# Performance work log

Measured on AMD Instinct MI355X. Metric: run time of the kernel, lower is better.

Reference implementation:

```python
import jax, jax.numpy as jnp
import numpy as np

B, N, C_IN = 128, 49, 2048   # batch, spatial tokens, backbone channels
G, D, H = 256, 768, 8        # query groups, decoder dim, heads
FF = 2048                    # feedforward dim
NUM_CLASSES = 12547
DUP = 50                     # int(12547/256 + 0.999)


def setup_inputs() -> dict:
    key = jax.random.key(0)
    ks = jax.random.split(key, 24)

    def rn(k, shape, std):
        return jax.random.normal(k, shape, dtype=jnp.float32) * std

    inp = {
        "x": rn(ks[0], (B, N, C_IN), 1.0),
        # embed_standart: Linear(2048 -> 768)
        "W_embed": rn(ks[1], (C_IN, D), (2.0 / (C_IN + D)) ** 0.5),
        "b_embed": jnp.zeros((D,), jnp.float32),
        # query embedding (frozen nn.Embedding weight)
        "query": rn(ks[2], (G, D), 1.0),
        # cross-attention projections (MultiheadAttention, 8 heads)
        "Wq": rn(ks[3], (D, D), D ** -0.5), "bq": jnp.zeros((D,), jnp.float32),
        "Wk": rn(ks[4], (D, D), D ** -0.5), "bk": jnp.zeros((D,), jnp.float32),
        "Wv": rn(ks[5], (D, D), D ** -0.5), "bv": jnp.zeros((D,), jnp.float32),
        "Wo": rn(ks[6], (D, D), D ** -0.5), "bo": jnp.zeros((D,), jnp.float32),
        # layer norms
        "g1": jnp.ones((D,), jnp.float32), "beta1": jnp.zeros((D,), jnp.float32),
        "g2": jnp.ones((D,), jnp.float32), "beta2": jnp.zeros((D,), jnp.float32),
        "g3": jnp.ones((D,), jnp.float32), "beta3": jnp.zeros((D,), jnp.float32),
        # FFN
        "W1": rn(ks[7], (D, FF), (2.0 / (D + FF)) ** 0.5), "b1": jnp.zeros((FF,), jnp.float32),
        "W2": rn(ks[8], (FF, D), (2.0 / (D + FF)) ** 0.5), "b2": jnp.zeros((D,), jnp.float32),
        # GroupFC: 256 stacked [768, 50] xavier-normal matrices + class bias
        "Wg": rn(ks[9], (G, D, DUP), (2.0 / (D + DUP)) ** 0.5),
        "bg": jnp.zeros((NUM_CLASSES,), jnp.float32),
    }
    return inp


def _layer_norm(x, g, b, eps=1e-5):
    m = x.mean(-1, keepdims=True)
    v = ((x - m) ** 2).mean(-1, keepdims=True)
    return (x - m) * jax.lax.rsqrt(v + eps) * g + b


def reference(x, W_embed, b_embed, query, Wq, bq, Wk, bk, Wv, bv, Wo, bo,
              g1, beta1, g2, beta2, g3, beta3, W1, b1, W2, b2, Wg, bg):
    hd = D // H
    # embed_standart + relu  -> memory [B, N, D]
    mem = jax.nn.relu(jnp.einsum('bnc,cd->bnd', x, W_embed) + b_embed)
    bs = x.shape[0]
    tgt = jnp.broadcast_to(query[None], (bs, G, D))

    # TransformerDecoderLayerOptimal (eval mode, dropout=identity):
    # tgt = norm1(tgt + dropout1(tgt)) == norm1(2*tgt)
    t = _layer_norm(tgt + tgt, g1, beta1)

    # cross-attention over memory
    q = (t @ Wq + bq).reshape(bs, G, H, hd)
    k = (mem @ Wk + bk).reshape(bs, N, H, hd)
    v = (mem @ Wv + bv).reshape(bs, N, H, hd)
    scores = jnp.einsum('bghd,bnhd->bhgn', q, k) / jnp.asarray(hd, t.dtype) ** 0.5
    attn = jax.nn.softmax(scores, axis=-1)
    o = jnp.einsum('bhgn,bnhd->bghd', attn, v).reshape(bs, G, D)
    o = o @ Wo + bo
    t = _layer_norm(t + o, g2, beta2)

    # FFN
    ff = jax.nn.relu(t @ W1 + b1) @ W2 + b2
    h = _layer_norm(t + ff, g3, beta3)  # [B, G, D]

    # GroupFC: fused grouped GEMM instead of the 256-iteration Python loop
    out_extrap = jnp.einsum('bgd,gdf->bgf', h, Wg)  # [B, G, DUP]
    logits = out_extrap.reshape(bs, G * DUP)[:, :NUM_CLASSES] + bg
    return logits
```

## Files before the change

### kernel.cpp

```cpp
#include <hip/hip_runtime.h>

#define Bn    128
#define Ntok  49
#define CIN   2048
#define Gq    256
#define Dm    768
#define Hh    8
#define HDd   96
#define FFd   2048
#define NCLS  12547
#define DUPn  50

typedef __attribute__((ext_vector_type(8))) short short8;
typedef __attribute__((ext_vector_type(4))) short short4v;
typedef __attribute__((ext_vector_type(4))) float floatx4;

__device__ __forceinline__ unsigned short f2bf(float f) {
  unsigned u = __builtin_bit_cast(unsigned, f);
  u += 0x7fffu + ((u >> 16) & 1u);
  return (unsigned short)(u >> 16);
}
__device__ __forceinline__ float bf2f(unsigned short h) {
  return __builtin_bit_cast(float, (unsigned)h << 16);
}

__device__ __forceinline__ void gl_lds16(const unsigned short* g, unsigned short* l) {
  __builtin_amdgcn_global_load_lds(
      (__attribute__((address_space(1))) void*)g,
      (__attribute__((address_space(3))) void*)l, 16, 0, 0);
}

__global__ __launch_bounds__(256)
void gemm_bt(const unsigned short* __restrict__ A,
             const unsigned short* __restrict__ Bt,
             const float* __restrict__ bias,
             unsigned short* __restrict__ C,
             int M, int N, int K, int relu)
{
  __shared__ unsigned short As[128 * 32];
  __shared__ unsigned short Bs[128 * 32];

  const int tid  = threadIdx.x;
  const int m0   = blockIdx.y << 7;
  const int n0   = blockIdx.x << 7;
  const int wave = tid >> 6, lane = tid & 63;
  const int wm   = (wave >> 1) << 6;
  const int wn   = (wave & 1) << 6;
  const int l16  = lane & 15, quad = lane >> 4;

  const int srow = (wave << 5) + (lane >> 2);
  const int scol = (lane & 3) << 3;
  const unsigned short* gA = A  + (size_t)(m0 + srow) * K + scol;
  const unsigned short* gB = Bt + (size_t)(n0 + srow) * K + scol;
  const size_t rstep = (size_t)16 * K;
  unsigned short* lA = &As[wave << 10];
  unsigned short* lB = &Bs[wave << 10];

  floatx4 acc[4][4];
  const floatx4 zero4 = {0.f, 0.f, 0.f, 0.f};
#pragma unroll
  for (int i = 0; i < 4; ++i)
#pragma unroll
    for (int j = 0; j < 4; ++j) acc[i][j] = zero4;

  for (int k0 = 0; k0 < K; k0 += 32) {
    gl_lds16(gA + k0,         lA);
    gl_lds16(gA + k0 + rstep, lA + 512);
    gl_lds16(gB + k0,         lB);
    gl_lds16(gB + k0 + rstep, lB + 512);
    __syncthreads();

    short8 a[4], b[4];
#pragma unroll
    for (int i = 0; i < 4; ++i)
      a[i] = *(const short8*)&As[(wm + (i << 4) + l16) * 32 + (quad << 3)];
#pragma unroll
    for (int j = 0; j < 4; ++j)
      b[j] = *(const short8*)&Bs[(wn + (j << 4) + l16) * 32 + (quad << 3)];
#pragma unroll
    for (int i = 0; i < 4; ++i)
#pragma unroll
      for (int j = 0; j < 4; ++j)
        acc[i][j] = __builtin_amdgcn_mfma_f32_16x16x32_bf16(a[i], b[j], acc[i][j], 0, 0, 0);
    __syncthreads();
  }

#pragma unroll
  for (int j = 0; j < 4; ++j) {
    const int col = n0 + wn + (j << 4) + l16;
    const float bv = bias[col];
#pragma unroll
    for (int i = 0; i < 4; ++i) {
      const int rbase = m0 + wm + (i << 4) + (quad << 2);
#pragma unroll
      for (int r = 0; r < 4; ++r) {
        float v = acc[i][j][r] + bv;
        if (relu) v = fmaxf(v, 0.f);
        C[(size_t)(rbase + r) * N + col] = f2bf(v);
      }
    }
  }
}

__global__ __launch_bounds__(256)
void cvt_k(const float* __restrict__ in, unsigned short* __restrict__ out, int n4)
{
  const int i = blockIdx.x * 256 + threadIdx.x;
  if (i < n4) {
    floatx4 v = ((const floatx4*)in)[i];
    short4v s;
    s.x = (short)f2bf(v.x); s.y = (short)f2bf(v.y);
    s.z = (short)f2bf(v.z); s.w = (short)f2bf(v.w);
    ((short4v*)out)[i] = s;
  }
}

__global__ __launch_bounds__(256)
void transcvt_k(const float* __restrict__ in, unsigned short* __restrict__ out,
                int K, int N)
{
  __shared__ float tile[32][33];
  const int nb = blockIdx.x << 5, kb = blockIdx.y << 5;
  const int tx = threadIdx.x & 31, ty = threadIdx.x >> 5;
#pragma unroll
  for (int i = 0; i < 4; ++i)
    tile[ty + (i << 3)][tx] = in[(size_t)(kb + ty + (i << 3)) * N + nb + tx];
  __syncthreads();
#pragma unroll
  for (int i = 0; i < 4; ++i)
    out[(size_t)(nb + ty + (i << 3)) * K + kb + tx] = f2bf(tile[tx][ty + (i << 3)]);
}

__global__ __launch_bounds__(256)
void wg_trans_k(const float* __restrict__ Wg, unsigned short* __restrict__ out)
{
  __shared__ float tile[32][33];
  const int g  = blockIdx.z;
  const int nb = blockIdx.x << 5, kb = blockIdx.y << 5;
  const int tx = threadIdx.x & 31, ty = threadIdx.x >> 5;
  const float* in = Wg + (size_t)g * Dm * DUPn;
#pragma unroll
  for (int i = 0; i < 4; ++i) {
    const int f = nb + tx;
    tile[ty + (i << 3)][tx] =
        (f < DUPn) ? in[(size_t)(kb + ty + (i << 3)) * DUPn + f] : 0.f;
  }
  __syncthreads();
  unsigned short* o = out + (size_t)g * 64 * Dm;
#pragma unroll
  for (int i = 0; i < 4; ++i)
    o[(size_t)(nb + ty + (i << 3)) * Dm + kb + tx] = f2bf(tile[tx][ty + (i << 3)]);
}

__global__ __launch_bounds__(256)
void groupfc_k(const unsigned short* __restrict__ hb, const unsigned short* __restrict__ wgT,
               const float* __restrict__ bg, float* __restrict__ out,
               int b0, int bcnt)
{
  __shared__ unsigned short As[128 * 32];
  __shared__ unsigned short Bs[64 * 32];

  const int g    = blockIdx.x;
  const int tid  = threadIdx.x;
  const int wave = tid >> 6, lane = tid & 63;
  const int wm   = (wave & 1) << 6;
  const int wn   = (wave >> 1) << 5;
  const int l16  = lane & 15, quad = lane >> 4;

  const int srow = (wave << 5) + (lane >> 2);
  const int brow = (wave << 4) + (lane >> 2);
  const int scol = (lane & 3) << 3;
  const unsigned short* gA = hb + ((size_t)srow * Gq + g) * Dm + scol;
  const unsigned short* gB = wgT + (size_t)g * 64 * Dm + (size_t)brow * Dm + scol;
  const size_t rstepA = (size_t)16 * Gq * Dm;
  unsigned short* lA = &As[wave << 10];
  unsigned short* lB = &Bs[wave << 9];

  floatx4 acc[4][2];
  const floatx4 zero4 = {0.f, 0.f, 0.f, 0.f};
#pragma unroll
  for (int i = 0; i < 4; ++i)
#pragma unroll
    for (int j = 0; j < 2; ++j) acc[i][j] = zero4;

  for (int k0 = 0; k0 < Dm; k0 += 32) {
    gl_lds16(gA + k0,          lA);
    gl_lds16(gA + k0 + rstepA, lA + 512);
    gl_lds16(gB + k0,          lB);
    __syncthreads();

    short8 a[4], b[2];
#pragma unroll
    for (int i = 0; i < 4; ++i)
      a[i] = *(const short8*)&As[(wm + (i << 4) + l16) * 32 + (quad << 3)];
#pragma unroll
    for (int j = 0; j < 2; ++j)
      b[j] = *(const short8*)&Bs[(wn + (j << 4) + l16) * 32 + (quad << 3)];
#pragma unroll
    for (int i = 0; i < 4; ++i)
#pragma unroll
      for (int j = 0; j < 2; ++j)
        acc[i][j] = __builtin_amdgcn_mfma_f32_16x16x32_bf16(a[i], b[j], acc[i][j], 0, 0, 0);
    __syncthreads();
  }

#pragma unroll
  for (int j = 0; j < 2; ++j) {
    const int f = wn + (j << 4) + l16;
    const int col = g * DUPn + f;
    const bool okf = (f < DUPn) && (col < NCLS);
    const float bv = okf ? bg[col] : 0.f;
#pragma unroll
    for (int i = 0; i < 4; ++i) {
      const int bb = wm + (i << 4) + (quad << 2);
#pragma unroll
      for (int r = 0; r < 4; ++r) {
        if (okf && bb + r < bcnt)
          out[(size_t)(b0 + bb + r) * NCLS + col] = acc[i][j][r] + bv;
      }
    }
  }
}

__global__ __launch_bounds__(256)
void ln_query_k(const float* __restrict__ query, const float* __restrict__ gamma,
                const float* __restrict__ beta, unsigned short* __restrict__ out)
{
  const unsigned row = blockIdx.x;
  const float* p = query + (size_t)row * Dm;
  const int tid = threadIdx.x;

  float v[3];
#pragma unroll
  for (int i = 0; i < 3; ++i) v[i] = 2.f * p[tid + (i << 8)];

  float s1 = v[0] + v[1] + v[2];
  float s2 = v[0]*v[0] + v[1]*v[1] + v[2]*v[2];
#pragma unroll
  for (int off = 32; off; off >>= 1) {
    s1 += __shfl_down(s1, off, 64);
    s2 += __shfl_down(s2, off, 64);
  }
  __shared__ float r1[4], r2[4];
  const int wave = tid >> 6, lane = tid & 63;
  if (lane == 0) { r1[wave] = s1; r2[wave] = s2; }
  __syncthreads();
  s1 = r1[0] + r1[1] + r1[2] + r1[3];
  s2 = r2[0] + r2[1] + r2[2] + r2[3];
  const float mean = s1 * (1.f / Dm);
  const float var  = s2 * (1.f / Dm) - mean * mean;
  const float inv  = rsqrtf(var + 1e-5f);
#pragma unroll
  for (int i = 0; i < 3; ++i) {
    const int c = tid + (i << 8);
    out[(size_t)row * Dm + c] = f2bf((v[i] - mean) * inv * gamma[c] + beta[c]);
  }
}

__global__ __launch_bounds__(256)
void ln_k(const unsigned short* __restrict__ in1, const unsigned short* __restrict__ in2,
          unsigned in2mask, const float* __restrict__ gamma,
          const float* __restrict__ beta, unsigned short* __restrict__ out)
{
  const unsigned row = blockIdx.x;
  const unsigned short* p1 = in1 + (size_t)row * Dm;
  const unsigned short* p2 = in2 + (size_t)(row & in2mask) * Dm;
  const int tid = threadIdx.x;

  float v[3];
#pragma unroll
  for (int i = 0; i < 3; ++i) v[i] = bf2f(p1[tid + (i << 8)]) + bf2f(p2[tid + (i << 8)]);

  float s1 = v[0] + v[1] + v[2];
  float s2 = v[0]*v[0] + v[1]*v[1] + v[2]*v[2];
#pragma unroll
  for (int off = 32; off; off >>= 1) {
    s1 += __shfl_down(s1, off, 64);
    s2 += __shfl_down(s2, off, 64);
  }
  __shared__ float r1[4], r2[4];
  const int wave = tid >> 6, lane = tid & 63;
  if (lane == 0) { r1[wave] = s1; r2[wave] = s2; }
  __syncthreads();
  s1 = r1[0] + r1[1] + r1[2] + r1[3];
  s2 = r2[0] + r2[1] + r2[2] + r2[3];
  const float mean = s1 * (1.f / Dm);
  const float var  = s2 * (1.f / Dm) - mean * mean;
  const float inv  = rsqrtf(var + 1e-5f);
#pragma unroll
  for (int i = 0; i < 3; ++i) {
    const int c = tid + (i << 8);
    out[(size_t)row * Dm + c] = f2bf((v[i] - mean) * inv * gamma[c] + beta[c]);
  }
}

__global__ __launch_bounds__(256)
void attn_k(const unsigned short* __restrict__ qall, const unsigned short* __restrict__ kbuf,
            const unsigned short* __restrict__ vbuf, unsigned short* __restrict__ attno,
            int b0)
{
  __shared__ unsigned short smem[24576];
  unsigned short* Vt = smem;
  unsigned short* Ks = smem + 6144;
  unsigned short* Ps = smem + 6144;

  const int h = blockIdx.x, bl = blockIdx.y;
  const int b = b0 + bl;
  const int tid  = threadIdx.x;
  const int wave = tid >> 6, lane = tid & 63;
  const int l16  = lane & 15, quad = lane >> 4;
  const int wm   = wave << 6;

  const size_t kvbase = (size_t)b * Ntok * Dm + h * HDd;

  for (int s = tid; s < 64 * 12; s += 256) {
    const int n = s / 12, c8 = (s - n * 12) << 3;
    short8 v = {0, 0, 0, 0, 0, 0, 0, 0};
    if (n < Ntok) v = *(const short8*)(kbuf + kvbase + (size_t)n * Dm + c8);
    *(short8*)&Ks[n * 96 + c8] = v;
  }
  for (int s = tid; s < Ntok * 12; s += 256) {
    const int n = s / 12, c8 = (s - n * 12) << 3;
    short8 v = *(const short8*)(vbuf + kvbase + (size_t)n * Dm + c8);
#pragma unroll
    for (int j = 0; j < 8; ++j) Vt[(c8 + j) * 64 + n] = v[j];
  }
  for (int s = tid; s < 96 * 15; s += 256) {
    const int d = s / 15, n = Ntok + (s - d * 15);
    Vt[d * 64 + n] = 0;
  }
  __syncthreads();

  floatx4 acc[4][4];
  const floatx4 zero4 = {0.f, 0.f, 0.f, 0.f};
#pragma unroll
  for (int i = 0; i < 4; ++i)
#pragma unroll
    for (int j = 0; j < 4; ++j) acc[i][j] = zero4;

#pragma unroll
  for (int kk = 0; kk < 96; kk += 32) {
    short8 a[4], bf[4];
#pragma unroll
    for (int i = 0; i < 4; ++i)
      a[i] = *(const short8*)(qall + (size_t)(wm + (i << 4) + l16) * Dm + h * HDd + kk + (quad << 3));
#pragma unroll
    for (int j = 0; j < 4; ++j)
      bf[j] = *(const short8*)&Ks[((j << 4) + l16) * 96 + kk + (quad << 3)];
#pragma unroll
    for (int i = 0; i < 4; ++i)
#pragma unroll
      for (int j = 0; j < 4; ++j)
        acc[i][j] = __builtin_amdgcn_mfma_f32_16x16x32_bf16(a[i], bf[j], acc[i][j], 0, 0, 0);
  }
  __syncthreads();

  const float scale = 0.10206207261596575f;
#pragma unroll
  for (int i = 0; i < 4; ++i) {
#pragma unroll
    for (int r = 0; r < 4; ++r) {
      float s0 = acc[i][0][r], s1 = acc[i][1][r];
      float s2 = acc[i][2][r], s3 = acc[i][3][r];
      if (l16 > 0) s3 = -1e30f;
      float mx = fmaxf(fmaxf(s0, s1), fmaxf(s2, s3));
      mx = fmaxf(mx, __shfl_xor(mx, 1));
      mx = fmaxf(mx, __shfl_xor(mx, 2));
      mx = fmaxf(mx, __shfl_xor(mx, 4));
      mx = fmaxf(mx, __shfl_xor(mx, 8));
      const float e0 = __expf((s0 - mx) * scale);
      const float e1 = __expf((s1 - mx) * scale);
      const float e2 = __expf((s2 - mx) * scale);
      const float e3 = __expf((s3 - mx) * scale);
      float sum = e0 + e1 + e2 + e3;
      sum += __shfl_xor(sum, 1);
      sum += __shfl_xor(sum, 2);
      sum += __shfl_xor(sum, 4);
      sum += __shfl_xor(sum, 8);
      const float rs = 1.f / sum;
      const int m = wm + (i << 4) + (quad << 2) + r;
      Ps[m * 72 +      l16] = f2bf(e0 * rs);
      Ps[m * 72 + 16 + l16] = f2bf(e1 * rs);
      Ps[m * 72 + 32 + l16] = f2bf(e2 * rs);
      Ps[m * 72 + 48 + l16] = f2bf(e3 * rs);
    }
  }
  __syncthreads();

  floatx4 o[4][6];
#pragma unroll
  for (int i = 0; i < 4; ++i)
#pragma unroll
    for (int j = 0; j < 6; ++j) o[i][j] = zero4;

#pragma unroll
  for (int kk = 0; kk < 64; kk += 32) {
    short8 a[4], bf[6];
#pragma unroll
    for (int i = 0; i < 4; ++i)
      a[i] = *(const short8*)&Ps[(wm + (i << 4) + l16) * 72 + kk + (quad << 3)];
#pragma unroll
    for (int j = 0; j < 6; ++j)
      bf[j] = *(const short8*)&Vt[((j << 4) + l16) * 64 + kk + (quad << 3)];
#pragma unroll
    for (int i = 0; i < 4; ++i)
#pragma unroll
      for (int j = 0; j < 6; ++j)
        o[i][j] = __builtin_amdgcn_mfma_f32_16x16x32_bf16(a[i], bf[j], o[i][j], 0, 0, 0);
  }

#pragma unroll
  for (int j = 0; j < 6; ++j) {
    const int d = (j << 4) + l16;
#pragma unroll
    for (int i = 0; i < 4; ++i) {
      const int mb = wm + (i << 4) + (quad << 2);
#pragma unroll
      for (int r = 0; r < 4; ++r)
        attno[((size_t)bl * Gq + mb + r) * Dm + h * HDd + d] = f2bf(o[i][j][r]);
    }
  }
}


static inline void gemm_launch(const unsigned short* A, const unsigned short* Bt,
                               const float* bias, unsigned short* C,
                               int M, int N, int K, int relu, hipStream_t s) {
  dim3 grid(N >> 7, M >> 7);
  gemm_bt<<<grid, 256, 0, s>>>(A, Bt, bias, C, M, N, K, relu);
}

extern "C" void kernel_launch(void* const* d_in, const int* in_sizes, int n_in,
                              void* d_out, int out_size, void* d_ws, size_t ws_size,
                              hipStream_t stream) {
  const float* x       = (const float*)d_in[0];
  const float* W_embed = (const float*)d_in[1];
  const float* b_embed = (const float*)d_in[2];
  const float* query   = (const float*)d_in[3];
  const float* Wq = (const float*)d_in[4];  const float* bq  = (const float*)d_in[5];
  const float* Wk = (const float*)d_in[6];  const float* bk  = (const float*)d_in[7];
  const float* Wv = (const float*)d_in[8];  const float* bv  = (const float*)d_in[9];
  const float* Wo = (const float*)d_in[10]; const float* bo  = (const float*)d_in[11];
  const float* g1 = (const float*)d_in[12]; const float* be1 = (const float*)d_in[13];
  const float* g2 = (const float*)d_in[14]; const float* be2 = (const float*)d_in[15];
  const float* g3 = (const float*)d_in[16]; const float* be3 = (const float*)d_in[17];
  const float* W1 = (const float*)d_in[18]; const float* b1  = (const float*)d_in[19];
  const float* W2 = (const float*)d_in[20]; const float* b2  = (const float*)d_in[21];
  const float* Wg = (const float*)d_in[22]; const float* bg  = (const float*)d_in[23];
  float* out = (float*)d_out;

  unsigned short* ws    = (unsigned short*)d_ws;
  unsigned short* tbuf  = ws;
  unsigned short* qall  = tbuf  + 196608;
  unsigned short* mem   = qall  + 196608;
  unsigned short* kbuf  = mem   + 4816896;
  unsigned short* vbuf  = kbuf  + 4816896;
  unsigned short* xbf   = vbuf  + 4816896;
  unsigned short* wembT = xbf   + 12845056;
  unsigned short* wqT   = wembT + 1572864;
  unsigned short* wkT   = wqT   + 589824;
  unsigned short* wvT   = wkT   + 589824;
  unsigned short* woT   = wvT   + 589824;
  unsigned short* w1T   = woT   + 589824;
  unsigned short* w2T   = w1T   + 1572864;
  unsigned short* attc  = w2T   + 1572864;
  unsigned short* wgT   = xbf;

  const size_t fixed_elems = 34766848;
  int CB = 128;
  while (CB > 4 && (fixed_elems + (size_t)CB * 1114112) * 2 > ws_size) CB >>= 1;
  const size_t cstride = (size_t)CB * 196608;
  unsigned short* oprc = attc + cstride;
  unsigned short* t2c  = oprc + cstride;
  unsigned short* ff1c = t2c  + cstride;
  unsigned short* ff2c = attc;
  unsigned short* hc   = oprc;

  cvt_k<<<(Bn * Ntok * CIN / 4 + 255) / 256, 256, 0, stream>>>(x, xbf, Bn * Ntok * CIN / 4);
  transcvt_k<<<dim3(Dm / 32, CIN / 32), 256, 0, stream>>>(W_embed, wembT, CIN, Dm);
  transcvt_k<<<dim3(Dm / 32, Dm / 32),  256, 0, stream>>>(Wq, wqT, Dm, Dm);
  transcvt_k<<<dim3(Dm / 32, Dm / 32),  256, 0, stream>>>(Wk, wkT, Dm, Dm);
  transcvt_k<<<dim3(Dm / 32, Dm / 32),  256, 0, stream>>>(Wv, wvT, Dm, Dm);
  transcvt_k<<<dim3(Dm / 32, Dm / 32),  256, 0, stream>>>(Wo, woT, Dm, Dm);
  transcvt_k<<<dim3(FFd / 32, Dm / 32), 256, 0, stream>>>(W1, w1T, Dm, FFd);
  transcvt_k<<<dim3(Dm / 32, FFd / 32), 256, 0, stream>>>(W2, w2T, FFd, Dm);

  ln_query_k<<<Gq, 256, 0, stream>>>(query, g1, be1, tbuf);
  gemm_launch(tbuf, wqT, bq, qall, Gq, Dm, Dm, 0, stream);
  gemm_launch(xbf, wembT, b_embed, mem, Bn * Ntok, Dm, CIN, 1, stream);
  wg_trans_k<<<dim3(2, Dm / 32, 251), 256, 0, stream>>>(Wg, wgT);
  gemm_launch(mem, wkT, bk, kbuf, Bn * Ntok, Dm, Dm, 0, stream);
  gemm_launch(mem, wvT, bv, vbuf, Bn * Ntok, Dm, Dm, 0, stream);

  for (int b0 = 0; b0 < Bn; b0 += CB) {
    const int rows = CB * Gq;
    attn_k<<<dim3(Hh, CB), 256, 0, stream>>>(qall, kbuf, vbuf, attc, b0);
    gemm_launch(attc, woT, bo, oprc, rows, Dm, Dm, 0, stream);
    ln_k<<<rows, 256, 0, stream>>>(oprc, tbuf, 255u, g2, be2, t2c);
    gemm_launch(t2c, w1T, b1, ff1c, rows, FFd, Dm, 1, stream);
    gemm_launch(ff1c, w2T, b2, ff2c, rows, Dm, FFd, 0, stream);
    ln_k<<<rows, 256, 0, stream>>>(ff2c, t2c, 0xFFFFFFFFu, g3, be3, hc);
    groupfc_k<<<251, 256, 0, stream>>>(hc, wgT, bg, out, b0, CB);
  }
}
```

Baseline: 821.0 us.

## Double GEMM K-tile, fuse K/V projections, and batch weight prep launches

The bf16 MFMA GEMM now stages 64-wide K tiles instead of 32, doing two MFMA sub-steps per tile. This halves the number of barrier pairs and global-to-LDS rounds per output tile. The K and V projections become one GEMM with N=1536, using the already-contiguous transposed wk/wv weights and a concatenated bias, and attention reads an interleaved KV buffer. The seven weight transpose-convert launches are merged into one kernel that dispatches blocks by index. The 128-byte LDS row stride may raise bank conflicts on the fragment reads, and the larger LDS footprint can reduce occupancy.

New measurement: 858.2 us. +4.5%, slower.

```diff
diff --git a/kernel.cpp b/kernel.cpp
--- a/kernel.cpp
+++ b/kernel.cpp
@@ -37,8 +37,8 @@
              unsigned short* __restrict__ C,
              int M, int N, int K, int relu)
 {
-  __shared__ unsigned short As[128 * 32];
-  __shared__ unsigned short Bs[128 * 32];
+  __shared__ unsigned short As[128 * 64];
+  __shared__ unsigned short Bs[128 * 64];
 
   const int tid  = threadIdx.x;
   const int m0   = blockIdx.y << 7;
@@ -48,13 +48,13 @@
   const int wn   = (wave & 1) << 6;
   const int l16  = lane & 15, quad = lane >> 4;
 
-  const int srow = (wave << 5) + (lane >> 2);
-  const int scol = (lane & 3) << 3;
+  const int srow = (wave << 5) + (lane >> 3);
+  const int scol = (lane & 7) << 3;
   const unsigned short* gA = A  + (size_t)(m0 + srow) * K + scol;
   const unsigned short* gB = Bt + (size_t)(n0 + srow) * K + scol;
-  const size_t rstep = (size_t)16 * K;
-  unsigned short* lA = &As[wave << 10];
-  unsigned short* lB = &Bs[wave << 10];
+  const size_t rstep8 = (size_t)8 * K;
+  unsigned short* lA = &As[(wave << 5) * 64];
+  unsigned short* lB = &Bs[(wave << 5) * 64];
 
   floatx4 acc[4][4];
   const floatx4 zero4 = {0.f, 0.f, 0.f, 0.f};
@@ -63,25 +63,29 @@
 #pragma unroll
     for (int j = 0; j < 4; ++j) acc[i][j] = zero4;
 
-  for (int k0 = 0; k0 < K; k0 += 32) {
-    gl_lds16(gA + k0,         lA);
-    gl_lds16(gA + k0 + rstep, lA + 512);
-    gl_lds16(gB + k0,         lB);
-    gl_lds16(gB + k0 + rstep, lB + 512);
+  for (int k0 = 0; k0 < K; k0 += 64) {
+#pragma unroll
+    for (int p = 0; p < 4; ++p) {
+      gl_lds16(gA + k0 + p * rstep8, lA + (p << 9));
+      gl_lds16(gB + k0 + p * rstep8, lB + (p << 9));
+    }
     __syncthreads();
 
-    short8 a[4], b[4];
-#pragma unroll
-    for (int i = 0; i < 4; ++i)
-      a[i] = *(const short8*)&As[(wm + (i << 4) + l16) * 32 + (quad << 3)];
-#pragma unroll
-    for (int j = 0; j < 4; ++j)
-      b[j] = *(const short8*)&Bs[(wn + (j << 4) + l16) * 32 + (quad << 3)];
-#pragma unroll
-    for (int i = 0; i < 4; ++i)
+#pragma unroll
+    for (int ks = 0; ks < 2; ++ks) {
+      short8 a[4], b[4];
+#pragma unroll
+      for (int i = 0; i < 4; ++i)
+        a[i] = *(const short8*)&As[(wm + (i << 4) + l16) * 64 + (ks << 5) + (quad << 3)];
 #pragma unroll
       for (int j = 0; j < 4; ++j)
-        acc[i][j] = __builtin_amdgcn_mfma_f32_16x16x32_bf16(a[i], b[j], acc[i][j], 0, 0, 0);
+        b[j] = *(const short8*)&Bs[(wn + (j << 4) + l16) * 64 + (ks << 5) + (quad << 3)];
+#pragma unroll
+      for (int i = 0; i < 4; ++i)
+#pragma unroll
+        for (int j = 0; j < 4; ++j)
+          acc[i][j] = __builtin_amdgcn_mfma_f32_16x16x32_bf16(a[i], b[j], acc[i][j], 0, 0, 0);
+    }
     __syncthreads();
   }
 
@@ -115,12 +119,25 @@
   }
 }
 
-__global__ __launch_bounds__(256)
-void transcvt_k(const float* __restrict__ in, unsigned short* __restrict__ out,
-                int K, int N)
+struct WPrep {
+  const float* src[7];
+  unsigned short* dst[7];
+  int K[7], N[7], nb[7];
+};
+
+__global__ __launch_bounds__(256)
+void wprep_k(WPrep p)
 {
   __shared__ float tile[32][33];
-  const int nb = blockIdx.x << 5, kb = blockIdx.y << 5;
+  int id = blockIdx.x, e = 0, base = 0;
+  while (e < 7 && id >= base + p.nb[e]) { base += p.nb[e]; ++e; }
+  if (e >= 7) return;
+  const int local = id - base;
+  const int K = p.K[e], N = p.N[e];
+  const int nbx = N >> 5;
+  const int nb = (local % nbx) << 5, kb = (local / nbx) << 5;
+  const float* in = p.src[e];
+  unsigned short* out = p.dst[e];
   const int tx = threadIdx.x & 31, ty = threadIdx.x >> 5;
 #pragma unroll
   for (int i = 0; i < 4; ++i)
@@ -129,6 +146,15 @@
 #pragma unroll
   for (int i = 0; i < 4; ++i)
     out[(size_t)(nb + ty + (i << 3)) * K + kb + tx] = f2bf(tile[tx][ty + (i << 3)]);
+}
+
+__global__ __launch_bounds__(256)
+void bkv_k(const float* __restrict__ bk, const float* __restrict__ bv,
+           float* __restrict__ o)
+{
+  const int i = blockIdx.x * 256 + threadIdx.x;
+  if (i < Dm) o[i] = bk[i];
+  else if (i < 2 * Dm) o[i] = bv[i - Dm];
 }
 
 __global__ __launch_bounds__(256)
@@ -295,9 +321,8 @@
 }
 
 __global__ __launch_bounds__(256)
-void attn_k(const unsigned short* __restrict__ qall, const unsigned short* __restrict__ kbuf,
-            const unsigned short* __restrict__ vbuf, unsigned short* __restrict__ attno,
-            int b0)
+void attn_k(const unsigned short* __restrict__ qall, const unsigned short* __restrict__ kv,
+            unsigned short* __restrict__ attno, int b0)
 {
   __shared__ unsigned short smem[24576];
   unsigned short* Vt = smem;
@@ -311,17 +336,17 @@
   const int l16  = lane & 15, quad = lane >> 4;
   const int wm   = wave << 6;
 
-  const size_t kvbase = (size_t)b * Ntok * Dm + h * HDd;
+  const size_t kvbase = (size_t)b * Ntok * 1536 + h * HDd;
 
   for (int s = tid; s < 64 * 12; s += 256) {
     const int n = s / 12, c8 = (s - n * 12) << 3;
     short8 v = {0, 0, 0, 0, 0, 0, 0, 0};
-    if (n < Ntok) v = *(const short8*)(kbuf + kvbase + (size_t)n * Dm + c8);
+    if (n < Ntok) v = *(const short8*)(kv + kvbase + (size_t)n * 1536 + c8);
     *(short8*)&Ks[n * 96 + c8] = v;
   }
   for (int s = tid; s < Ntok * 12; s += 256) {
     const int n = s / 12, c8 = (s - n * 12) << 3;
-    short8 v = *(const short8*)(vbuf + kvbase + (size_t)n * Dm + c8);
+    short8 v = *(const short8*)(kv + kvbase + (size_t)n * 1536 + Dm + c8);
 #pragma unroll
     for (int j = 0; j < 8; ++j) Vt[(c8 + j) * 64 + n] = v[j];
   }
@@ -453,9 +478,8 @@
   unsigned short* tbuf  = ws;
   unsigned short* qall  = tbuf  + 196608;
   unsigned short* mem   = qall  + 196608;
-  unsigned short* kbuf  = mem   + 4816896;
-  unsigned short* vbuf  = kbuf  + 4816896;
-  unsigned short* xbf   = vbuf  + 4816896;
+  unsigned short* kvbuf = mem   + 4816896;
+  unsigned short* xbf   = kvbuf + 9633792;
   unsigned short* wembT = xbf   + 12845056;
   unsigned short* wqT   = wembT + 1572864;
   unsigned short* wkT   = wqT   + 589824;
@@ -463,10 +487,11 @@
   unsigned short* woT   = wvT   + 589824;
   unsigned short* w1T   = woT   + 589824;
   unsigned short* w2T   = w1T   + 1572864;
-  unsigned short* attc  = w2T   + 1572864;
+  float*          bkv   = (float*)(w2T + 1572864);
+  unsigned short* attc  = w2T   + 1572864 + 3072;
   unsigned short* wgT   = xbf;
 
-  const size_t fixed_elems = 34766848;
+  const size_t fixed_elems = 34769920;
   int CB = 128;
   while (CB > 4 && (fixed_elems + (size_t)CB * 1114112) * 2 > ws_size) CB >>= 1;
   const size_t cstride = (size_t)CB * 196608;
@@ -477,24 +502,30 @@
   unsigned short* hc   = oprc;
 
   cvt_k<<<(Bn * Ntok * CIN / 4 + 255) / 256, 256, 0, stream>>>(x, xbf, Bn * Ntok * CIN / 4);
-  transcvt_k<<<dim3(Dm / 32, CIN / 32), 256, 0, stream>>>(W_embed, wembT, CIN, Dm);
-  transcvt_k<<<dim3(Dm / 32, Dm / 32),  256, 0, stream>>>(Wq, wqT, Dm, Dm);
-  transcvt_k<<<dim3(Dm / 32, Dm / 32),  256, 0, stream>>>(Wk, wkT, Dm, Dm);
-  transcvt_k<<<dim3(Dm / 32, Dm / 32),  256, 0, stream>>>(Wv, wvT, Dm, Dm);
-  transcvt_k<<<dim3(Dm / 32, Dm / 32),  256, 0, stream>>>(Wo, woT, Dm, Dm);
-  transcvt_k<<<dim3(FFd / 32, Dm / 32), 256, 0, stream>>>(W1, w1T, Dm, FFd);
-  transcvt_k<<<dim3(Dm / 32, FFd / 32), 256, 0, stream>>>(W2, w2T, FFd, Dm);
+  {
+    WPrep p;
+    p.src[0] = W_embed; p.dst[0] = wembT; p.K[0] = CIN; p.N[0] = Dm;
+    p.src[1] = Wq;      p.dst[1] = wqT;   p.K[1] = Dm;  p.N[1] = Dm;
+    p.src[2] = Wk;      p.dst[2] = wkT;   p.K[2] = Dm;  p.N[2] = Dm;
+    p.src[3] = Wv;      p.dst[3] = wvT;   p.K[3] = Dm;  p.N[3] = Dm;
+    p.src[4] = Wo;      p.dst[4] = woT;   p.K[4] = Dm;  p.N[4] = Dm;
+    p.src[5] = W1;      p.dst[5] = w1T;   p.K[5] = Dm;  p.N[5] = FFd;
+    p.src[6] = W2;      p.dst[6] = w2T;   p.K[6] = FFd; p.N[6] = Dm;
+    int total = 0;
+    for (int e = 0; e < 7; ++e) { p.nb[e] = (p.N[e] >> 5) * (p.K[e] >> 5); total += p.nb[e]; }
+    wprep_k<<<total, 256, 0, stream>>>(p);
+  }
+  bkv_k<<<6, 256, 0, stream>>>(bk, bv, bkv);
 
   ln_query_k<<<Gq, 256, 0, stream>>>(query, g1, be1, tbuf);
   gemm_launch(tbuf, wqT, bq, qall, Gq, Dm, Dm, 0, stream);
   gemm_launch(xbf, wembT, b_embed, mem, Bn * Ntok, Dm, CIN, 1, stream);
   wg_trans_k<<<dim3(2, Dm / 32, 251), 256, 0, stream>>>(Wg, wgT);
-  gemm_launch(mem, wkT, bk, kbuf, Bn * Ntok, Dm, Dm, 0, stream);
-  gemm_launch(mem, wvT, bv, vbuf, Bn * Ntok, Dm, Dm, 0, stream);
+  gemm_launch(mem, wkT, bkv, kvbuf, Bn * Ntok, 2 * Dm, Dm, 0, stream);
 
   for (int b0 = 0; b0 < Bn; b0 += CB) {
     const int rows = CB * Gq;
-    attn_k<<<dim3(Hh, CB), 256, 0, stream>>>(qall, kbuf, vbuf, attc, b0);
+    attn_k<<<dim3(Hh, CB), 256, 0, stream>>>(qall, kvbuf, attc, b0);
     gemm_launch(attc, woT, bo, oprc, rows, Dm, Dm, 0, stream);
     ln_k<<<rows, 256, 0, stream>>>(oprc, tbuf, 255u, g2, be2, t2c);
     gemm_launch(t2c, w1T, b1, ff1c, rows, FFd, Dm, 1, stream);
```
